# Kernel tuning notes

Hardware: AMD Instinct MI355X
Metric: run time of the kernel (lower is better)

The kernel has to match this reference:

```python
import jax, jax.numpy as jnp
import numpy as np

GAMMA = 0.99
LMBDA = 0.95
SHAPE = (8192, 256, 4, 1)  # (batch, steps, agents, 1)


def setup_inputs() -> dict:
    key = jax.random.key(0)
    k1, k2, k3, k4 = jax.random.split(key, 4)
    reward = jax.random.normal(k1, SHAPE, dtype=jnp.float32)
    # sparse binary termination flags (as float, matching terminated.float())
    terminated = (jax.random.uniform(k2, SHAPE) < 0.01).astype(jnp.float32)
    value = jax.random.normal(k3, SHAPE, dtype=jnp.float32)
    next_value = jax.random.normal(k4, SHAPE, dtype=jnp.float32)
    return {"reward": reward, "terminated": terminated,
            "value": value, "next_value": next_value}


def _gae(reward, terminated, value, next_value):
    not_done = 1.0 - terminated
    # delta_t = r_t + gamma * V(s_{t+1}) * not_done_t - V(s_t), all steps at once
    delta = reward + GAMMA * next_value * not_done - value  # (B, T, ...)

    # time-major for the scan: (T, B, ...)
    delta_t = jnp.moveaxis(delta, 1, 0)
    nd_t = jnp.moveaxis(not_done, 1, 0)

    def step(gae, x):
        d, nd = x
        gae = d + GAMMA * LMBDA * nd * gae
        return gae, gae

    init = jnp.zeros(delta_t.shape[1:], dtype=delta.dtype)
    # reverse=True: backward-time recurrence, outputs aligned to original order
    _, adv_t = jax.lax.scan(step, init, (delta_t, nd_t), reverse=True)
    advantages = jnp.moveaxis(adv_t, 0, 1)  # back to (B, T, ...)
    returns = advantages + value
    return advantages, returns


def reference(reward, terminated, value, next_value):
    return _gae(reward, terminated, value, next_value)
```

## Files before the change

### kernel.cpp

```cpp
#include <hip/hip_runtime.h>


#define GAMMA 0.99f
#define LMBDA 0.95f

constexpr int T = 256;
constexpr float K0 = GAMMA * LMBDA;

__global__ __launch_bounds__(256, 8) void gae_scan_kernel(
    const float* __restrict__ reward,
    const float* __restrict__ terminated,
    const float* __restrict__ value,
    const float* __restrict__ next_value,
    float* __restrict__ adv_out,
    float* __restrict__ ret_out)
{
    __shared__ float bufD[4][16 * 64];
    __shared__ unsigned char bufC[4][16 * 64];

    const int w    = threadIdx.x >> 6;
    const int lane = threadIdx.x & 63;
    const int b    = blockIdx.x * 4 + w;

    float* __restrict__ D_ = bufD[w];
    unsigned char* __restrict__ C_ = bufC[w];

    float4 v4[4];
#pragma unroll
    for (int q = 0; q < 4; ++q) {
        const int f  = 64 * q + lane;
        const int gi = b * 256 + f;
        const float4 r  = ((const float4*)reward)[gi];
        const float4 tm = ((const float4*)terminated)[gi];
        const float4 v  = ((const float4*)value)[gi];
        const float4 nv = ((const float4*)next_value)[gi];
        v4[q] = v;

        const int s    = 255 - f;
        const int row  = s & 15;
        const int col  = (4 * (s >> 4) + 4 * row) & 63;
        const int addr = row * 64 + col;

        float4 d4;
        d4.x = r.x + GAMMA * nv.x * (1.0f - tm.x) - v.x;
        d4.y = r.y + GAMMA * nv.y * (1.0f - tm.y) - v.y;
        d4.z = r.z + GAMMA * nv.z * (1.0f - tm.z) - v.z;
        d4.w = r.w + GAMMA * nv.w * (1.0f - tm.w) - v.w;
        uchar4 c4;
        c4.x = (tm.x == 0.0f) ? (unsigned char)1 : (unsigned char)0;
        c4.y = (tm.y == 0.0f) ? (unsigned char)1 : (unsigned char)0;
        c4.z = (tm.z == 0.0f) ? (unsigned char)1 : (unsigned char)0;
        c4.w = (tm.w == 0.0f) ? (unsigned char)1 : (unsigned char)0;
        *((float4*)&D_[addr]) = d4;
        *((uchar4*)&C_[addr]) = c4;
    }
    __syncthreads();

    const int tc = lane >> 2;
    const int a  = lane & 3;

    float d[16];
    unsigned int mask = 0;
#pragma unroll
    for (int j = 0; j < 16; ++j) {
        const int col = (4 * tc + 4 * j + a) & 63;
        d[j] = D_[j * 64 + col];
        mask |= ((unsigned int)C_[j * 64 + col]) << j;
    }

    float D = d[0];
    float K = (mask & 1u) ? K0 : 0.0f;
#pragma unroll
    for (int j = 1; j < 16; ++j) {
        const float cj = ((mask >> j) & 1u) ? K0 : 0.0f;
        D = d[j] + cj * D;
        K = cj * K;
    }

#pragma unroll
    for (int s2 = 1; s2 < 16; s2 <<= 1) {
        const float pD = __shfl_up(D, (unsigned)(4 * s2), 64);
        const float pK = __shfl_up(K, (unsigned)(4 * s2), 64);
        if (tc >= s2) { D = D + K * pD; K = K * pK; }
    }

    float x = __shfl_up(D, 4u, 64);
    if (tc == 0) x = 0.0f;

    float g = x;
#pragma unroll
    for (int j = 0; j < 16; ++j) {
        const float cj = ((mask >> j) & 1u) ? K0 : 0.0f;
        g = d[j] + cj * g;
        const int col = (4 * tc + 4 * j + a) & 63;
        D_[j * 64 + col] = g;
    }
    __syncthreads();

#pragma unroll
    for (int q = 0; q < 4; ++q) {
        const int f   = 64 * q + lane;
        const int s   = 255 - f;
        const int row = s & 15;
        const int col = (4 * (s >> 4) + 4 * row) & 63;
        const float4 g4 = *((const float4*)&D_[row * 64 + col]);

        const int gi = b * 256 + f;
        ((float4*)adv_out)[gi] = g4;
        float4 rt;
        rt.x = g4.x + v4[q].x;
        rt.y = g4.y + v4[q].y;
        rt.z = g4.z + v4[q].z;
        rt.w = g4.w + v4[q].w;
        ((float4*)ret_out)[gi] = rt;
    }
}

extern "C" void kernel_launch(void* const* d_in, const int* in_sizes, int n_in,
                              void* d_out, int out_size, void* d_ws, size_t ws_size,
                              hipStream_t stream) {
    const float* reward     = (const float*)d_in[0];
    const float* terminated = (const float*)d_in[1];
    const float* value      = (const float*)d_in[2];
    const float* next_value = (const float*)d_in[3];

    const int B = 8192;
    const int n_elem = B * T * 4;
    float* adv = (float*)d_out;
    float* ret = adv + n_elem;

    gae_scan_kernel<<<B / 4, 256, 0, stream>>>(reward, terminated, value,
                                               next_value, adv, ret);
}
```

Before: 190.4 us.

## Process two batch rows per wave with prefetched loads and nontemporal stores

Each wave now handles two batch rows. The global loads for the second row are issued before the scan of the first, so memory latency overlaps with LDS scan work, and the grid is halved. Block-wide __syncthreads is replaced by per-wave s_waitcnt lgkmcnt(0), since each wave uses only its own LDS slice. Output stores become nontemporal and the condition bytes are packed into a single 32-bit store. The cost is higher register pressure (launch bounds lowered to 4 waves per SIMD) and reliance on wave-local LDS ordering without a barrier.

```diff
diff --git a/kernel.cpp b/kernel.cpp
--- a/kernel.cpp
+++ b/kernel.cpp
@@ -4,68 +4,69 @@
 #define GAMMA 0.99f
 #define LMBDA 0.95f
 
-constexpr int T = 256;
+typedef float f32x4 __attribute__((ext_vector_type(4)));
+typedef unsigned char u8;
+
 constexpr float K0 = GAMMA * LMBDA;
 
-__global__ __launch_bounds__(256, 8) void gae_scan_kernel(
-    const float* __restrict__ reward,
-    const float* __restrict__ terminated,
-    const float* __restrict__ value,
-    const float* __restrict__ next_value,
-    float* __restrict__ adv_out,
-    float* __restrict__ ret_out)
+__device__ __forceinline__ void issue_loads(
+    const f32x4* __restrict__ R4, const f32x4* __restrict__ T4,
+    const f32x4* __restrict__ V4, const f32x4* __restrict__ N4,
+    int b, int lane, f32x4 r[4], f32x4 tm[4], f32x4 v[4], f32x4 nv[4])
 {
-    __shared__ float bufD[4][16 * 64];
-    __shared__ unsigned char bufC[4][16 * 64];
-
-    const int w    = threadIdx.x >> 6;
-    const int lane = threadIdx.x & 63;
-    const int b    = blockIdx.x * 4 + w;
-
-    float* __restrict__ D_ = bufD[w];
-    unsigned char* __restrict__ C_ = bufC[w];
-
-    float4 v4[4];
 #pragma unroll
     for (int q = 0; q < 4; ++q) {
-        const int f  = 64 * q + lane;
-        const int gi = b * 256 + f;
-        const float4 r  = ((const float4*)reward)[gi];
-        const float4 tm = ((const float4*)terminated)[gi];
-        const float4 v  = ((const float4*)value)[gi];
-        const float4 nv = ((const float4*)next_value)[gi];
-        v4[q] = v;
+        const int gi = b * 256 + 64 * q + lane;
+        r[q]  = R4[gi];
+        tm[q] = T4[gi];
+        v[q]  = V4[gi];
+        nv[q] = N4[gi];
+    }
+}
 
+__device__ __forceinline__ void phaseA(
+    float* __restrict__ D_, u8* __restrict__ C_, int lane,
+    const f32x4 r[4], const f32x4 tm[4], const f32x4 nv[4], const f32x4 v[4])
+{
+#pragma unroll
+    for (int q = 0; q < 4; ++q) {
+        const int f    = 64 * q + lane;
         const int s    = 255 - f;
         const int row  = s & 15;
         const int col  = (4 * (s >> 4) + 4 * row) & 63;
         const int addr = row * 64 + col;
 
-        float4 d4;
-        d4.x = r.x + GAMMA * nv.x * (1.0f - tm.x) - v.x;
-        d4.y = r.y + GAMMA * nv.y * (1.0f - tm.y) - v.y;
-        d4.z = r.z + GAMMA * nv.z * (1.0f - tm.z) - v.z;
-        d4.w = r.w + GAMMA * nv.w * (1.0f - tm.w) - v.w;
-        uchar4 c4;
-        c4.x = (tm.x == 0.0f) ? (unsigned char)1 : (unsigned char)0;
-        c4.y = (tm.y == 0.0f) ? (unsigned char)1 : (unsigned char)0;
-        c4.z = (tm.z == 0.0f) ? (unsigned char)1 : (unsigned char)0;
-        c4.w = (tm.w == 0.0f) ? (unsigned char)1 : (unsigned char)0;
-        *((float4*)&D_[addr]) = d4;
-        *((uchar4*)&C_[addr]) = c4;
+        f32x4 d4;
+        d4.x = r[q].x + GAMMA * nv[q].x * (1.0f - tm[q].x) - v[q].x;
+        d4.y = r[q].y + GAMMA * nv[q].y * (1.0f - tm[q].y) - v[q].y;
+        d4.z = r[q].z + GAMMA * nv[q].z * (1.0f - tm[q].z) - v[q].z;
+        d4.w = r[q].w + GAMMA * nv[q].w * (1.0f - tm[q].w) - v[q].w;
+        const unsigned pk = (tm[q].x == 0.0f ? 0x00000001u : 0u)
+                          | (tm[q].y == 0.0f ? 0x00000100u : 0u)
+                          | (tm[q].z == 0.0f ? 0x00010000u : 0u)
+                          | (tm[q].w == 0.0f ? 0x01000000u : 0u);
+        *((f32x4*)&D_[addr])    = d4;
+        *((unsigned*)&C_[addr]) = pk;
     }
-    __syncthreads();
+}
+
+__device__ __forceinline__ void scan_store(
+    float* __restrict__ D_, const u8* __restrict__ C_,
+    int lane, int b, const f32x4 v4[4],
+    f32x4* __restrict__ adv4, f32x4* __restrict__ ret4)
+{
+    asm volatile("s_waitcnt lgkmcnt(0)" ::: "memory");
 
     const int tc = lane >> 2;
     const int a  = lane & 3;
 
     float d[16];
-    unsigned int mask = 0;
+    unsigned mask = 0;
 #pragma unroll
     for (int j = 0; j < 16; ++j) {
         const int col = (4 * tc + 4 * j + a) & 63;
         d[j] = D_[j * 64 + col];
-        mask |= ((unsigned int)C_[j * 64 + col]) << j;
+        mask |= ((unsigned)C_[j * 64 + col]) << j;
     }
 
     float D = d[0];
@@ -95,7 +96,7 @@
         const int col = (4 * tc + 4 * j + a) & 63;
         D_[j * 64 + col] = g;
     }
-    __syncthreads();
+    asm volatile("s_waitcnt lgkmcnt(0)" ::: "memory");
 
 #pragma unroll
     for (int q = 0; q < 4; ++q) {
@@ -103,17 +104,55 @@
         const int s   = 255 - f;
         const int row = s & 15;
         const int col = (4 * (s >> 4) + 4 * row) & 63;
-        const float4 g4 = *((const float4*)&D_[row * 64 + col]);
+        const f32x4 g4 = *((const f32x4*)&D_[row * 64 + col]);
 
         const int gi = b * 256 + f;
-        ((float4*)adv_out)[gi] = g4;
-        float4 rt;
-        rt.x = g4.x + v4[q].x;
-        rt.y = g4.y + v4[q].y;
-        rt.z = g4.z + v4[q].z;
-        rt.w = g4.w + v4[q].w;
-        ((float4*)ret_out)[gi] = rt;
+        __builtin_nontemporal_store(g4, &adv4[gi]);
+        const f32x4 rt = g4 + v4[q];
+        __builtin_nontemporal_store(rt, &ret4[gi]);
     }
+    asm volatile("" ::: "memory");
+}
+
+__global__ __launch_bounds__(256, 4) void gae_scan_kernel(
+    const float* __restrict__ reward,
+    const float* __restrict__ terminated,
+    const float* __restrict__ value,
+    const float* __restrict__ next_value,
+    float* __restrict__ adv_out,
+    float* __restrict__ ret_out)
+{
+    __shared__ float bufD[4][16 * 64];
+    __shared__ u8    bufC[4][16 * 64];
+
+    const int w    = threadIdx.x >> 6;
+    const int lane = threadIdx.x & 63;
+    const int wid  = blockIdx.x * 4 + w;
+
+    float* __restrict__ D_ = bufD[w];
+    u8*    __restrict__ C_ = bufC[w];
+
+    const f32x4* R4 = (const f32x4*)reward;
+    const f32x4* T4 = (const f32x4*)terminated;
+    const f32x4* V4 = (const f32x4*)value;
+    const f32x4* N4 = (const f32x4*)next_value;
+    f32x4* adv4 = (f32x4*)adv_out;
+    f32x4* ret4 = (f32x4*)ret_out;
+
+    const int b0 = wid;
+    const int b1 = wid + 4096;
+
+    f32x4 r0[4], t0[4], v0[4], n0[4];
+    issue_loads(R4, T4, V4, N4, b0, lane, r0, t0, v0, n0);
+    phaseA(D_, C_, lane, r0, t0, n0, v0);
+
+    f32x4 r1[4], t1[4], v1[4], n1[4];
+    issue_loads(R4, T4, V4, N4, b1, lane, r1, t1, v1, n1);
+
+    scan_store(D_, C_, lane, b0, v0, adv4, ret4);
+
+    phaseA(D_, C_, lane, r1, t1, n1, v1);
+    scan_store(D_, C_, lane, b1, v1, adv4, ret4);
 }
 
 extern "C" void kernel_launch(void* const* d_in, const int* in_sizes, int n_in,
@@ -125,10 +164,10 @@
     const float* next_value = (const float*)d_in[3];
 
     const int B = 8192;
-    const int n_elem = B * T * 4;
+    const int n_elem = B * 256 * 4;
     float* adv = (float*)d_out;
     float* ret = adv + n_elem;
 
-    gae_scan_kernel<<<B / 4, 256, 0, stream>>>(reward, terminated, value,
+    gae_scan_kernel<<<B / 8, 256, 0, stream>>>(reward, terminated, value,
                                                next_value, adv, ret);
 }
```

New measurement: 194.9 us. +2.4%, slower.
